# Optimization experiments

Measured on AMD Instinct MI355X. Metric: run time of the kernel, lower is better.

The kernel has to match this reference:

```python
import jax, jax.numpy as jnp
import numpy as np
import math

B, S, IN, D, H, L, DFF = 8, 512, 32, 512, 8, 6, 2048
DK = D // H
LN_EPS = 1e-5
KL_EPS = 1e-8


def _pos_encoding(seq_len, d_model):
    pe = np.zeros((seq_len, d_model), dtype=np.float32)
    pos = np.arange(seq_len, dtype=np.float32)[:, None]
    div = np.exp(np.arange(0, d_model, 2, dtype=np.float32) * (-math.log(10000.0) / d_model))
    pe[:, 0::2] = np.sin(pos * div)
    pe[:, 1::2] = np.cos(pos * div)
    return jnp.asarray(pe)


def setup_inputs() -> dict:
    key = jax.random.key(0)
    ks = iter(jax.random.split(key, 32))
    g = lambda shape: jax.random.normal(next(ks), shape, dtype=jnp.float32) * 0.02
    return {
        'x': jax.random.normal(next(ks), (B, S, IN), dtype=jnp.float32),
        'W_in': g((IN, D)), 'b_in': jnp.zeros((D,), jnp.float32),
        'pe': _pos_encoding(S, D),
        'Wq': g((L, D, D)), 'Wk': g((L, D, D)), 'Wv': g((L, D, D)),
        'Wo': g((L, D, D)), 'bo': jnp.zeros((L, D), jnp.float32),
        'W1': g((L, D, DFF)), 'b1': jnp.zeros((L, DFF), jnp.float32),
        'W2': g((L, DFF, D)), 'b2': jnp.zeros((L, D), jnp.float32),
        'ln1_g': jnp.ones((L, D), jnp.float32), 'ln1_b': jnp.zeros((L, D), jnp.float32),
        'ln2_g': jnp.ones((L, D), jnp.float32), 'ln2_b': jnp.zeros((L, D), jnp.float32),
        'W_out': g((D, IN)), 'b_out': jnp.zeros((IN,), jnp.float32),
        'Ws1': g((D, D // 2)), 'bs1': jnp.zeros((D // 2,), jnp.float32),
        'Ws2': g((D // 2, 1)), 'bs2': jnp.zeros((1,), jnp.float32),
    }


def _layernorm(v, gamma, beta):
    mu = v.mean(-1, keepdims=True)
    var = ((v - mu) ** 2).mean(-1, keepdims=True)
    return (v - mu) * jax.lax.rsqrt(var + LN_EPS) * gamma + beta


def reference(x, W_in, b_in, pe, Wq, Wk, Wv, Wo, bo, W1, b1, W2, b2,
              ln1_g, ln1_b, ln2_g, ln2_b, W_out, b_out, Ws1, bs1, Ws2, bs2):
    b, s, _ = x.shape
    h = x @ W_in + b_in + pe[None, :s, :]
    total_assoc = jnp.zeros((b, s), x.dtype)
    scale = 1.0 / math.sqrt(DK)
    prior = 1.0 / s + KL_EPS
    for l in range(L):
        # QKV: [b, h, s, dk]
        Q = (h @ Wq[l]).reshape(b, s, H, DK).transpose(0, 2, 1, 3)
        K = (h @ Wk[l]).reshape(b, s, H, DK).transpose(0, 2, 1, 3)
        V = (h @ Wv[l]).reshape(b, s, H, DK).transpose(0, 2, 1, 3)
        scores = jnp.einsum('bhsk,bhtk->bhst', Q, K) * scale
        attn = jax.nn.softmax(scores, axis=-1)  # [b,h,s,s]
        ctx = jnp.einsum('bhst,bhtk->bhsk', attn, V)
        ctx = ctx.transpose(0, 2, 1, 3).reshape(b, s, D)
        attn_out = ctx @ Wo[l] + bo[l]
        # association discrepancy: KL(avg_attn || uniform prior) per query
        avg_attn = attn.mean(axis=1) + KL_EPS  # [b,s,s]
        total_assoc = total_assoc + (avg_attn * jnp.log(avg_attn / prior)).sum(-1)
        h = _layernorm(h + attn_out, ln1_g[l], ln1_b[l])
        ff = jax.nn.relu(h @ W1[l] + b1[l]) @ W2[l] + b2[l]
        h = _layernorm(h + ff, ln2_g[l], ln2_b[l])
    reconstruction = h @ W_out + b_out
    anomaly_scores = jax.nn.sigmoid(jax.nn.relu(h @ Ws1 + bs1) @ Ws2 + bs2)[..., 0]
    avg_association = total_assoc / L
    return reconstruction, anomaly_scores, avg_association
```

## Files before the change

kernel.cpp:

```cpp
#include <hip/hip_runtime.h>
#include <math.h>

typedef __attribute__((ext_vector_type(8))) short bf16x8;
typedef __attribute__((ext_vector_type(4))) float f32x4;
typedef __attribute__((ext_vector_type(4))) float float4v;

__device__ __forceinline__ short f2bf(float v) {
  union { float f; unsigned u; } x; x.f = v;
  unsigned r = x.u + 0x7fffu + ((x.u >> 16) & 1u);
  return (short)(r >> 16);
}

__device__ __forceinline__ float bf2f(unsigned short u) {
  union { unsigned u; float f; } x; x.u = ((unsigned)u) << 16;
  return x.f;
}

__device__ __forceinline__ void gld_lds16(const void* g, void* l) {
  __builtin_amdgcn_global_load_lds((const __attribute__((address_space(1))) void*)g,
                                   (__attribute__((address_space(3))) void*)l, 16, 0, 0);
}

__global__ __launch_bounds__(256) void transpose_bf(const float* __restrict__ src,
                                                    short* __restrict__ dst,
                                                    int R, int C, size_t sStride, size_t dStride) {
  __shared__ float t[32][33];
  src += blockIdx.z * sStride;
  dst += blockIdx.z * dStride;
  int tx = threadIdx.x & 31, ty = threadIdx.x >> 5;
  int c0 = blockIdx.x * 32, r0 = blockIdx.y * 32;
#pragma unroll
  for (int i = 0; i < 4; i++)
    t[ty + i * 8][tx] = src[(size_t)(r0 + ty + i * 8) * C + c0 + tx];
  __syncthreads();
#pragma unroll
  for (int i = 0; i < 4; i++)
    dst[(size_t)(c0 + ty + i * 8) * R + r0 + tx] = f2bf(t[tx][ty + i * 8]);
}

__global__ __launch_bounds__(256) void transpose_qkv(const float* __restrict__ Wq,
                                                     const float* __restrict__ Wk,
                                                     const float* __restrict__ Wv,
                                                     short* __restrict__ qkvt) {
  __shared__ float t[32][33];
  const int z = blockIdx.z;
  const int which = z / 6, l = z % 6;
  const float* src = (which == 0 ? Wq : which == 1 ? Wk : Wv) + (size_t)l * 262144;
  short* dst = qkvt + (size_t)l * 786432 + (size_t)which * 262144;
  int tx = threadIdx.x & 31, ty = threadIdx.x >> 5;
  int c0 = blockIdx.x * 32, r0 = blockIdx.y * 32;
#pragma unroll
  for (int i = 0; i < 4; i++)
    t[ty + i * 8][tx] = src[(size_t)(r0 + ty + i * 8) * 512 + c0 + tx];
  __syncthreads();
#pragma unroll
  for (int i = 0; i < 4; i++)
    dst[(size_t)(c0 + ty + i * 8) * 512 + r0 + tx] = f2bf(t[tx][ty + i * 8]);
}

__global__ void embed_kernel(const float* __restrict__ x, const float* __restrict__ W_in,
                             const float* __restrict__ b_in, const float* __restrict__ pe,
                             float* __restrict__ h, short* __restrict__ hbf) {
  int col = (blockIdx.x & 1) * 256 + threadIdx.x;
  int row = blockIdx.x >> 1;
  int s = row & 511;
  float a = b_in[col] + pe[s * 512 + col];
  const float* xr = x + (size_t)row * 32;
#pragma unroll
  for (int k = 0; k < 32; k++) a += xr[k] * W_in[k * 512 + col];
  h[(size_t)row * 512 + col] = a;
  hbf[(size_t)row * 512 + col] = f2bf(a);
}

template <int EPI, int BM, int BN, int BK>
__global__ __launch_bounds__(256) void gemm_bt(const short* __restrict__ A,
                                               const short* __restrict__ Bt,
                                               float* __restrict__ Cf, short* __restrict__ Cb,
                                               const float* __restrict__ bias,
                                               int M, int N, int K) {
  __shared__ short As[BM * BK];
  __shared__ short Bs[BN * BK];
  const int tid = threadIdx.x;
  const int wid = tid >> 6;
  const int lane = tid & 63;
  const int m0 = blockIdx.y * BM;
  const int n0 = blockIdx.x * BN;
  constexpr int WR = BM / 2, WC = BN / 2, FI = WR / 16, FJ = WC / 16, KK = BK / 32;
  const int wr = (wid >> 1) * WR;
  const int wc = (wid & 1) * WC;

  f32x4 acc[FI][FJ];
#pragma unroll
  for (int i = 0; i < FI; i++)
#pragma unroll
    for (int j = 0; j < FJ; j++)
#pragma unroll
      for (int q = 0; q < 4; q++) acc[i][j][q] = 0.0f;

  const short* aBase = A + (size_t)m0 * K;
  const short* bBase = Bt + (size_t)n0 * K;
  constexpr int RPC = 512 / BK;
  constexpr int CA = BM / RPC;
  constexpr int CT = (BM + BN) / RPC;
  const int rowL = lane / (64 / RPC);
  const int colE = (lane % (64 / RPC)) * 8;
  const int kg = (lane >> 4) * 8;
  const int r16 = lane & 15;

  for (int kt = 0; kt < K; kt += BK) {
    __syncthreads();
#pragma unroll
    for (int c = 0; c < CT / 4; ++c) {
      int s = c * 4 + wid;
      if (s < CA)
        gld_lds16(aBase + (size_t)(s * RPC + rowL) * K + kt + colE, As + s * 512);
      else
        gld_lds16(bBase + (size_t)((s - CA) * RPC + rowL) * K + kt + colE, Bs + (s - CA) * 512);
    }
    __syncthreads();
    bf16x8 af[FI][KK], bfr[FJ][KK];
#pragma unroll
    for (int i = 0; i < FI; i++)
#pragma unroll
      for (int kk = 0; kk < KK; kk++)
        af[i][kk] = *(const bf16x8*)&As[(wr + i * 16 + r16) * BK + kk * 32 + kg];
#pragma unroll
    for (int j = 0; j < FJ; j++)
#pragma unroll
      for (int kk = 0; kk < KK; kk++)
        bfr[j][kk] = *(const bf16x8*)&Bs[(wc + j * 16 + r16) * BK + kk * 32 + kg];
#pragma unroll
    for (int kk = 0; kk < KK; kk++)
#pragma unroll
      for (int i = 0; i < FI; i++)
#pragma unroll
        for (int j = 0; j < FJ; j++)
          acc[i][j] = __builtin_amdgcn_mfma_f32_16x16x32_bf16(af[i][kk], bfr[j][kk], acc[i][j], 0, 0, 0);
  }

  const int col16 = lane & 15;
  const int rowg = (lane >> 4) * 4;
#pragma unroll
  for (int i = 0; i < FI; i++) {
    int row = m0 + wr + i * 16 + rowg;
#pragma unroll
    for (int j = 0; j < FJ; j++) {
      int col = n0 + wc + j * 16 + col16;
      float bv = (EPI == 1 || EPI == 2 || EPI == 4) ? bias[col] : 0.0f;
#pragma unroll
      for (int q = 0; q < 4; q++) {
        float v = acc[i][j][q] + bv;
        if (EPI == 2) {
          v = fmaxf(v, 0.0f);
          Cb[(size_t)(row + q) * N + col] = f2bf(v);
        } else if (EPI == 5) {
          int rr = row + q;
          int sect = col >> 9, hh = (col >> 6) & 7, dk = col & 63;
          int bq = rr >> 9, tt = rr & 511;
          Cb[(((size_t)(sect * 64 + bq * 8 + hh)) * 512 + tt) * 64 + dk] = f2bf(v);
        } else if (EPI == 3 || EPI == 4) {
          Cb[(size_t)(row + q) * N + col] = f2bf(v);
        } else {
          Cf[(size_t)(row + q) * N + col] = v;
        }
      }
    }
  }
}

__global__ __launch_bounds__(256) void vt_kernel(const short* __restrict__ qh,
                                                 short* __restrict__ Vt) {
  __shared__ short t[32][34];
  const int bh = blockIdx.z;
  const int t0 = blockIdx.x * 32, d0 = blockIdx.y * 32;
  const int tx = threadIdx.x & 31, ty = threadIdx.x >> 5;
  const short* Vh = qh + (size_t)(128 + bh) * 512 * 64;
#pragma unroll
  for (int i = 0; i < 4; i++)
    t[ty + i * 8][tx] = Vh[(size_t)(t0 + ty + i * 8) * 64 + d0 + tx];
  __syncthreads();
#pragma unroll
  for (int i = 0; i < 4; i++)
    Vt[((size_t)bh * 64 + d0 + ty + i * 8) * 512 + t0 + tx] = t[tx][ty + i * 8];
}

__global__ __launch_bounds__(256) void smpv_kernel(const short* __restrict__ qh,
                                                   const short* __restrict__ Vt,
                                                   short* __restrict__ P,
                                                   short* __restrict__ ctxb) {
  __shared__ short Pl[32 * 512];
  __shared__ float red0[2][2][16];
  __shared__ float red1[2][2][16];
  const int bh = blockIdx.y, b = bh >> 3, h = bh & 7;
  const int q0 = blockIdx.x * 32;
  const int tid = threadIdx.x;
  const int wid = tid >> 6, lane = tid & 63;
  const int r16 = lane & 15, g = lane >> 4;
  const int qh_ = wid & 1, th_ = wid >> 1;

  const short* Qh = qh + ((size_t)bh * 512) * 64;
  const short* Kh = qh + ((size_t)(64 + bh) * 512) * 64;

  const short* qp = Qh + (size_t)(q0 + qh_ * 16 + r16) * 64 + g * 8;
  const bf16x8 qa0 = *(const bf16x8*)qp;
  const bf16x8 qa1 = *(const bf16x8*)(qp + 32);

  f32x4 acc[16];
#pragma unroll
  for (int tt = 0; tt < 16; ++tt) {
    const short* kp = Kh + (size_t)(th_ * 256 + tt * 16 + r16) * 64 + g * 8;
    bf16x8 kb0 = *(const bf16x8*)kp;
    bf16x8 kb1 = *(const bf16x8*)(kp + 32);
    f32x4 c = {0.f, 0.f, 0.f, 0.f};
    c = __builtin_amdgcn_mfma_f32_16x16x32_bf16(qa0, kb0, c, 0, 0, 0);
    c = __builtin_amdgcn_mfma_f32_16x16x32_bf16(qa1, kb1, c, 0, 0, 0);
    acc[tt] = c;
  }

  float mx[4] = {-1e30f, -1e30f, -1e30f, -1e30f};
#pragma unroll
  for (int tt = 0; tt < 16; ++tt)
#pragma unroll
    for (int r = 0; r < 4; ++r) mx[r] = fmaxf(mx[r], acc[tt][r]);
#pragma unroll
  for (int r = 0; r < 4; ++r)
#pragma unroll
    for (int m = 8; m; m >>= 1) mx[r] = fmaxf(mx[r], __shfl_xor(mx[r], m, 16));
  if (r16 == 0) {
#pragma unroll
    for (int r = 0; r < 4; ++r) red0[th_][qh_][g * 4 + r] = mx[r];
  }
  __syncthreads();
#pragma unroll
  for (int r = 0; r < 4; ++r) {
    int q = g * 4 + r;
    mx[r] = fmaxf(red0[0][qh_][q], red0[1][qh_][q]);
  }
  float sum[4] = {0.f, 0.f, 0.f, 0.f};
#pragma unroll
  for (int tt = 0; tt < 16; ++tt)
#pragma unroll
    for (int r = 0; r < 4; ++r) {
      float e = __expf((acc[tt][r] - mx[r]) * 0.125f);
      acc[tt][r] = e;
      sum[r] += e;
    }
#pragma unroll
  for (int r = 0; r < 4; ++r)
#pragma unroll
    for (int m = 8; m; m >>= 1) sum[r] += __shfl_xor(sum[r], m, 16);
  if (r16 == 0) {
#pragma unroll
    for (int r = 0; r < 4; ++r) red1[th_][qh_][g * 4 + r] = sum[r];
  }
  __syncthreads();

  char* plc = (char*)Pl;
#pragma unroll
  for (int r = 0; r < 4; ++r) {
    int q = qh_ * 16 + g * 4 + r;
    float inv = 1.0f / (red1[0][qh_][g * 4 + r] + red1[1][qh_][g * 4 + r]);
    int swz = (q & 7) << 4;
#pragma unroll
    for (int tt = 0; tt < 16; ++tt)
      *(short*)(plc + q * 1024 + (((th_ * 256 + tt * 16 + r16) * 2) ^ swz)) =
          f2bf(acc[tt][r] * inv);
  }
  __syncthreads();

  short* pg = P + ((size_t)bh * 512 + q0) * 512;
#pragma unroll
  for (int rr = 0; rr < 8; ++rr) {
    int q = wid * 8 + rr;
    bf16x8 v = *(const bf16x8*)(plc + q * 1024 + ((lane * 16) ^ ((q & 7) << 4)));
    *(bf16x8*)&pg[(size_t)q * 512 + lane * 8] = v;
  }

  f32x4 pacc[2];
#pragma unroll
  for (int j = 0; j < 2; ++j)
#pragma unroll
    for (int q = 0; q < 4; ++q) pacc[j][q] = 0.f;
  const short* vb = Vt + (size_t)bh * 64 * 512 + (size_t)(th_ * 32) * 512;
  const int qr = qh_ * 16 + r16;
  const int rswz = (qr & 7) << 4;
  for (int kt = 0; kt < 512; kt += 32) {
    bf16x8 af = *(const bf16x8*)(plc + qr * 1024 + (((kt + g * 8) * 2) ^ rswz));
#pragma unroll
    for (int j = 0; j < 2; ++j) {
      bf16x8 bfr = *(const bf16x8*)&vb[(size_t)(j * 16 + r16) * 512 + kt + g * 8];
      pacc[j] = __builtin_amdgcn_mfma_f32_16x16x32_bf16(af, bfr, pacc[j], 0, 0, 0);
    }
  }
#pragma unroll
  for (int j = 0; j < 2; ++j) {
    int col = h * 64 + th_ * 32 + j * 16 + r16;
#pragma unroll
    for (int q = 0; q < 4; ++q)
      ctxb[(size_t)(b * 512 + q0 + qh_ * 16 + g * 4 + q) * 512 + col] = f2bf(pacc[j][q]);
  }
}

template <int FIRST>
__global__ __launch_bounds__(256) void kl_kernel(const short* __restrict__ P,
                                                 float* __restrict__ assoc) {
  const int wid = threadIdx.x >> 6, lane = threadIdx.x & 63;
  const int row = blockIdx.x * 4 + wid;
  const int b = row >> 9, q = row & 511;
  const float prior = 1.0f / 512.0f + 1e-8f;
  float hs[8] = {0.f, 0.f, 0.f, 0.f, 0.f, 0.f, 0.f, 0.f};
#pragma unroll
  for (int h = 0; h < 8; ++h) {
    bf16x8 v = *(const bf16x8*)&P[(((size_t)(b * 8 + h)) * 512 + q) * 512 + lane * 8];
#pragma unroll
    for (int k = 0; k < 8; ++k) hs[k] += bf2f((unsigned short)v[k]);
  }
  float s = 0.f;
#pragma unroll
  for (int k = 0; k < 8; ++k) {
    float a = hs[k] * 0.125f + 1e-8f;
    s += a * __logf(a / prior);
  }
#pragma unroll
  for (int m = 32; m; m >>= 1) s += __shfl_xor(s, m, 64);
  if (lane == 0) assoc[row] = FIRST ? s : (assoc[row] + s);
}

__global__ __launch_bounds__(256) void ln_kernel(const float* __restrict__ hin,
                                                 const short* __restrict__ res,
                                                 const float* __restrict__ g,
                                                 const float* __restrict__ bta,
                                                 float* __restrict__ hout, short* __restrict__ hbf) {
  const int wid = threadIdx.x >> 6, lane = threadIdx.x & 63;
  const size_t row = (size_t)blockIdx.x * 4 + wid;
  const float* hp = hin + row * 512 + lane * 8;
  float4v a0 = *(const float4v*)hp;
  float4v a1 = *(const float4v*)(hp + 4);
  bf16x8 rv = *(const bf16x8*)(res + row * 512 + lane * 8);
  float v[8], s = 0.f, s2 = 0.f;
#pragma unroll
  for (int i = 0; i < 8; i++) {
    float base = (i < 4) ? a0[i] : a1[i - 4];
    v[i] = base + bf2f((unsigned short)rv[i]);
    s += v[i];
    s2 += v[i] * v[i];
  }
#pragma unroll
  for (int m = 32; m; m >>= 1) {
    s += __shfl_xor(s, m, 64);
    s2 += __shfl_xor(s2, m, 64);
  }
  float mu = s * (1.0f / 512.0f);
  float var = s2 * (1.0f / 512.0f) - mu * mu;
  float rs = rsqrtf(var + 1e-5f);
  const float* gp = g + lane * 8;
  const float* bp = bta + lane * 8;
  float4v o0, o1;
  bf16x8 ob;
#pragma unroll
  for (int i = 0; i < 8; i++) {
    float y = (v[i] - mu) * rs * gp[i] + bp[i];
    if (i < 4) o0[i] = y; else o1[i - 4] = y;
    ob[i] = f2bf(y);
  }
  float* op = hout + row * 512 + lane * 8;
  *(float4v*)op = o0;
  *(float4v*)(op + 4) = o1;
  *(bf16x8*)(hbf + row * 512 + lane * 8) = ob;
}

__global__ __launch_bounds__(256) void recon_mfma(const short* __restrict__ hbf,
                                                  const short* __restrict__ WoutT,
                                                  const float* __restrict__ bout,
                                                  float* __restrict__ out) {
  const int wid = threadIdx.x >> 6, lane = threadIdx.x & 63;
  const int r16 = lane & 15, kg = (lane >> 4) * 8;
  const int wbase = blockIdx.x * 128 + wid * 32;

  f32x4 acc[2][2];
#pragma unroll
  for (int i = 0; i < 2; i++)
#pragma unroll
    for (int j = 0; j < 2; j++)
#pragma unroll
      for (int q = 0; q < 4; q++) acc[i][j][q] = 0.0f;

  for (int kt = 0; kt < 512; kt += 32) {
    bf16x8 af[2], bfr[2];
#pragma unroll
    for (int i = 0; i < 2; i++)
      af[i] = *(const bf16x8*)&hbf[(size_t)(wbase + i * 16 + r16) * 512 + kt + kg];
#pragma unroll
    for (int j = 0; j < 2; j++)
      bfr[j] = *(const bf16x8*)&WoutT[(size_t)(j * 16 + r16) * 512 + kt + kg];
#pragma unroll
    for (int i = 0; i < 2; i++)
#pragma unroll
      for (int j = 0; j < 2; j++)
        acc[i][j] = __builtin_amdgcn_mfma_f32_16x16x32_bf16(af[i], bfr[j], acc[i][j], 0, 0, 0);
  }

  const int rowg = (lane >> 4) * 4;
#pragma unroll
  for (int i = 0; i < 2; i++)
#pragma unroll
    for (int j = 0; j < 2; j++) {
      int col = j * 16 + r16;
#pragma unroll
      for (int q = 0; q < 4; q++)
        out[(size_t)(wbase + i * 16 + rowg + q) * 32 + col] = acc[i][j][q] + bout[col];
    }
}

__global__ __launch_bounds__(256) void score2_kernel(const short* __restrict__ s1,
                                                     const float* __restrict__ Ws2,
                                                     const float* __restrict__ bs2,
                                                     const float* __restrict__ assoc,
                                                     float* __restrict__ outScore,
                                                     float* __restrict__ outAssoc) {
  const int wid = threadIdx.x >> 6, lane = threadIdx.x & 63;
  const int row = blockIdx.x * 4 + wid;
  const short* rp = &s1[(size_t)row * 256 + lane * 4];
  float d = 0.f;
#pragma unroll
  for (int e = 0; e < 4; e++) d += bf2f((unsigned short)rp[e]) * Ws2[lane * 4 + e];
#pragma unroll
  for (int m = 32; m; m >>= 1) d += __shfl_xor(d, m, 64);
  if (lane == 0) {
    outScore[row] = 1.f / (1.f + __expf(-(d + bs2[0])));
    outAssoc[row] = assoc[row] * (1.0f / 6.0f);
  }
}

extern "C" void kernel_launch(void* const* d_in, const int* in_sizes, int n_in,
                              void* d_out, int out_size, void* d_ws, size_t ws_size,
                              hipStream_t stream) {
  const float* x    = (const float*)d_in[0];
  const float* W_in = (const float*)d_in[1];
  const float* b_in = (const float*)d_in[2];
  const float* pe   = (const float*)d_in[3];
  const float* Wq   = (const float*)d_in[4];
  const float* Wk   = (const float*)d_in[5];
  const float* Wv   = (const float*)d_in[6];
  const float* Wo   = (const float*)d_in[7];
  const float* bo   = (const float*)d_in[8];
  const float* W1   = (const float*)d_in[9];
  const float* b1   = (const float*)d_in[10];
  const float* W2   = (const float*)d_in[11];
  const float* b2   = (const float*)d_in[12];
  const float* ln1g = (const float*)d_in[13];
  const float* ln1b = (const float*)d_in[14];
  const float* ln2g = (const float*)d_in[15];
  const float* ln2b = (const float*)d_in[16];
  const float* Wout = (const float*)d_in[17];
  const float* bout = (const float*)d_in[18];
  const float* Ws1  = (const float*)d_in[19];
  const float* bs1  = (const float*)d_in[20];
  const float* Ws2  = (const float*)d_in[21];
  const float* bs2  = (const float*)d_in[22];

  char* p = (char*)d_ws;
  auto alloc = [&](size_t bytes) {
    void* r = (void*)p;
    p += (bytes + 255) & ~(size_t)255;
    return r;
  };
  float* h     = (float*)alloc((size_t)4096 * 512 * 4);
  short* h_bf  = (short*)alloc((size_t)4096 * 512 * 2);
  short* qh    = (short*)alloc((size_t)4096 * 1536 * 2);
  short* aout  = (short*)alloc((size_t)4096 * 512 * 2);
  short* ctxb  = (short*)alloc((size_t)4096 * 512 * 2);
  short* ff1b  = (short*)alloc((size_t)4096 * 2048 * 2);
  short* ff2   = (short*)alloc((size_t)4096 * 512 * 2);
  float* assoc = (float*)alloc((size_t)4096 * 4);
  short* Pbuf  = (short*)alloc((size_t)64 * 512 * 512 * 2);
  short* Vt    = (short*)alloc((size_t)64 * 64 * 512 * 2);
  short* sc1   = (short*)alloc((size_t)4096 * 256 * 2);
  short* qkvt  = (short*)alloc((size_t)6 * 1536 * 512 * 2);
  short* wot   = (short*)alloc((size_t)6 * 512 * 512 * 2);
  short* w1t   = (short*)alloc((size_t)6 * 2048 * 512 * 2);
  short* w2t   = (short*)alloc((size_t)6 * 512 * 2048 * 2);
  short* ws1t  = (short*)alloc((size_t)256 * 512 * 2);
  short* woutT = (short*)alloc((size_t)32 * 512 * 2);

  transpose_qkv<<<dim3(16, 16, 18), 256, 0, stream>>>(Wq, Wk, Wv, qkvt);
  transpose_bf<<<dim3(16, 16, 6), 256, 0, stream>>>(Wo, wot, 512, 512, 262144, 262144);
  transpose_bf<<<dim3(64, 16, 6), 256, 0, stream>>>(W1, w1t, 512, 2048, 1048576, 1048576);
  transpose_bf<<<dim3(16, 64, 6), 256, 0, stream>>>(W2, w2t, 2048, 512, 1048576, 1048576);
  transpose_bf<<<dim3(8, 16, 1), 256, 0, stream>>>(Ws1, ws1t, 512, 256, 0, 0);
  transpose_bf<<<dim3(1, 16, 1), 256, 0, stream>>>(Wout, woutT, 512, 32, 0, 0);

  embed_kernel<<<8192, 256, 0, stream>>>(x, W_in, b_in, pe, h, h_bf);

  for (int l = 0; l < 6; ++l) {
    gemm_bt<5, 128, 128, 32><<<dim3(12, 32), 256, 0, stream>>>(
        h_bf, qkvt + (size_t)l * 786432, nullptr, qh, nullptr, 4096, 1536, 512);
    vt_kernel<<<dim3(16, 2, 64), 256, 0, stream>>>(qh, Vt);
    smpv_kernel<<<dim3(16, 64), 256, 0, stream>>>(qh, Vt, Pbuf, ctxb);
    if (l == 0)
      kl_kernel<1><<<1024, 256, 0, stream>>>(Pbuf, assoc);
    else
      kl_kernel<0><<<1024, 256, 0, stream>>>(Pbuf, assoc);
    gemm_bt<4, 64, 64, 32><<<dim3(8, 64), 256, 0, stream>>>(
        ctxb, wot + (size_t)l * 262144, nullptr, aout, bo + l * 512, 4096, 512, 512);
    ln_kernel<<<1024, 256, 0, stream>>>(h, aout, ln1g + l * 512, ln1b + l * 512, h, h_bf);
    gemm_bt<2, 128, 128, 32><<<dim3(16, 32), 256, 0, stream>>>(
        h_bf, w1t + (size_t)l * 1048576, nullptr, ff1b, b1 + l * 2048, 4096, 2048, 512);
    gemm_bt<4, 64, 64, 32><<<dim3(8, 64), 256, 0, stream>>>(
        ff1b, w2t + (size_t)l * 1048576, nullptr, ff2, b2 + l * 512, 4096, 512, 2048);
    ln_kernel<<<1024, 256, 0, stream>>>(h, ff2, ln2g + l * 512, ln2b + l * 512, h, h_bf);
  }

  float* out = (float*)d_out;
  recon_mfma<<<32, 256, 0, stream>>>(h_bf, woutT, bout, out);
  gemm_bt<2, 128, 128, 32><<<dim3(2, 32), 256, 0, stream>>>(h_bf, ws1t, nullptr, sc1, bs1,
                                                            4096, 256, 512);
  score2_kernel<<<1024, 256, 0, stream>>>(sc1, Ws2, bs2, assoc, out + 131072,
                                          out + 131072 + 4096);
}
```

Baseline: 864.7 us.

## Fuse prologue kernels, merge Wo GEMM with KL, drop fp32 residual stream

Merges all weight transposes and the embedding into one prologue launch, and runs the Wo projection GEMM and the KL association reduction as two block ranges of a single launch. The fp32 hidden-state copy is removed, so the residual and LayerNorm now read and write only the bf16 hidden buffer. The goal is fewer launches and less memory traffic. In exchange, residual accumulation happens in bf16 across six layers, which may reduce accuracy.

```diff
diff --git a/kernel.cpp b/kernel.cpp
--- a/kernel.cpp
+++ b/kernel.cpp
@@ -3,7 +3,6 @@
 
 typedef __attribute__((ext_vector_type(8))) short bf16x8;
 typedef __attribute__((ext_vector_type(4))) float f32x4;
-typedef __attribute__((ext_vector_type(4))) float float4v;
 
 __device__ __forceinline__ short f2bf(float v) {
   union { float f; unsigned u; } x; x.f = v;
@@ -21,14 +20,68 @@
                                    (__attribute__((address_space(3))) void*)l, 16, 0, 0);
 }
 
-__global__ __launch_bounds__(256) void transpose_bf(const float* __restrict__ src,
-                                                    short* __restrict__ dst,
-                                                    int R, int C, size_t sStride, size_t dStride) {
+__global__ __launch_bounds__(256) void prologue_kernel(
+    const float* __restrict__ x, const float* __restrict__ W_in, const float* __restrict__ b_in,
+    const float* __restrict__ pe, short* __restrict__ hbf,
+    const float* __restrict__ Wq, const float* __restrict__ Wk, const float* __restrict__ Wv,
+    const float* __restrict__ Wo, const float* __restrict__ W1, const float* __restrict__ W2,
+    const float* __restrict__ Ws1, const float* __restrict__ Wout,
+    short* __restrict__ qkvt, short* __restrict__ wot, short* __restrict__ w1t,
+    short* __restrict__ w2t, short* __restrict__ ws1t, short* __restrict__ woutT) {
   __shared__ float t[32][33];
-  src += blockIdx.z * sStride;
-  dst += blockIdx.z * dStride;
-  int tx = threadIdx.x & 31, ty = threadIdx.x >> 5;
-  int c0 = blockIdx.x * 32, r0 = blockIdx.y * 32;
+  const int tid = threadIdx.x;
+  int idx = blockIdx.x;
+  if (idx < 8192) {
+    int col = (idx & 1) * 256 + tid;
+    int row = idx >> 1;
+    int s = row & 511;
+    float a = b_in[col] + pe[s * 512 + col];
+    const float* xr = x + (size_t)row * 32;
+#pragma unroll
+    for (int k = 0; k < 32; k++) a += xr[k] * W_in[k * 512 + col];
+    hbf[(size_t)row * 512 + col] = f2bf(a);
+    return;
+  }
+  idx -= 8192;
+  const float* src;
+  short* dst;
+  int R, C, cx, cy;
+  if (idx < 4608) {
+    int z = idx >> 8, rem = idx & 255;
+    cx = rem & 15; cy = rem >> 4;
+    int which = z / 6, l = z % 6;
+    src = (which == 0 ? Wq : which == 1 ? Wk : Wv) + (size_t)l * 262144;
+    dst = qkvt + (size_t)l * 786432 + (size_t)which * 262144;
+    R = 512; C = 512;
+  } else if (idx < 6144) {
+    int j = idx - 4608;
+    int l = j >> 8, rem = j & 255;
+    cx = rem & 15; cy = rem >> 4;
+    src = Wo + (size_t)l * 262144; dst = wot + (size_t)l * 262144;
+    R = 512; C = 512;
+  } else if (idx < 12288) {
+    int j = idx - 6144;
+    int l = j >> 10, rem = j & 1023;
+    cx = rem & 63; cy = rem >> 6;
+    src = W1 + (size_t)l * 1048576; dst = w1t + (size_t)l * 1048576;
+    R = 512; C = 2048;
+  } else if (idx < 18432) {
+    int j = idx - 12288;
+    int l = j >> 10, rem = j & 1023;
+    cx = rem & 15; cy = rem >> 4;
+    src = W2 + (size_t)l * 1048576; dst = w2t + (size_t)l * 1048576;
+    R = 2048; C = 512;
+  } else if (idx < 18560) {
+    int j = idx - 18432;
+    cx = j & 7; cy = j >> 3;
+    src = Ws1; dst = ws1t; R = 512; C = 256;
+  } else {
+    int j = idx - 18560;
+    cx = 0; cy = j;
+    src = Wout; dst = woutT; R = 512; C = 32;
+  }
+  const int tx = tid & 31, ty = tid >> 5;
+  const int c0 = cx * 32, r0 = cy * 32;
 #pragma unroll
   for (int i = 0; i < 4; i++)
     t[ty + i * 8][tx] = src[(size_t)(r0 + ty + i * 8) * C + c0 + tx];
@@ -38,44 +91,10 @@
     dst[(size_t)(c0 + ty + i * 8) * R + r0 + tx] = f2bf(t[tx][ty + i * 8]);
 }
 
-__global__ __launch_bounds__(256) void transpose_qkv(const float* __restrict__ Wq,
-                                                     const float* __restrict__ Wk,
-                                                     const float* __restrict__ Wv,
-                                                     short* __restrict__ qkvt) {
-  __shared__ float t[32][33];
-  const int z = blockIdx.z;
-  const int which = z / 6, l = z % 6;
-  const float* src = (which == 0 ? Wq : which == 1 ? Wk : Wv) + (size_t)l * 262144;
-  short* dst = qkvt + (size_t)l * 786432 + (size_t)which * 262144;
-  int tx = threadIdx.x & 31, ty = threadIdx.x >> 5;
-  int c0 = blockIdx.x * 32, r0 = blockIdx.y * 32;
-#pragma unroll
-  for (int i = 0; i < 4; i++)
-    t[ty + i * 8][tx] = src[(size_t)(r0 + ty + i * 8) * 512 + c0 + tx];
-  __syncthreads();
-#pragma unroll
-  for (int i = 0; i < 4; i++)
-    dst[(size_t)(c0 + ty + i * 8) * 512 + r0 + tx] = f2bf(t[tx][ty + i * 8]);
-}
-
-__global__ void embed_kernel(const float* __restrict__ x, const float* __restrict__ W_in,
-                             const float* __restrict__ b_in, const float* __restrict__ pe,
-                             float* __restrict__ h, short* __restrict__ hbf) {
-  int col = (blockIdx.x & 1) * 256 + threadIdx.x;
-  int row = blockIdx.x >> 1;
-  int s = row & 511;
-  float a = b_in[col] + pe[s * 512 + col];
-  const float* xr = x + (size_t)row * 32;
-#pragma unroll
-  for (int k = 0; k < 32; k++) a += xr[k] * W_in[k * 512 + col];
-  h[(size_t)row * 512 + col] = a;
-  hbf[(size_t)row * 512 + col] = f2bf(a);
-}
-
 template <int EPI, int BM, int BN, int BK>
 __global__ __launch_bounds__(256) void gemm_bt(const short* __restrict__ A,
                                                const short* __restrict__ Bt,
-                                               float* __restrict__ Cf, short* __restrict__ Cb,
+                                               short* __restrict__ Cb,
                                                const float* __restrict__ bias,
                                                int M, int N, int K) {
   __shared__ short As[BM * BK];
@@ -146,7 +165,7 @@
 #pragma unroll
     for (int j = 0; j < FJ; j++) {
       int col = n0 + wc + j * 16 + col16;
-      float bv = (EPI == 1 || EPI == 2 || EPI == 4) ? bias[col] : 0.0f;
+      float bv = (EPI == 2 || EPI == 4) ? bias[col] : 0.0f;
 #pragma unroll
       for (int q = 0; q < 4; q++) {
         float v = acc[i][j][q] + bv;
@@ -158,10 +177,8 @@
           int sect = col >> 9, hh = (col >> 6) & 7, dk = col & 63;
           int bq = rr >> 9, tt = rr & 511;
           Cb[(((size_t)(sect * 64 + bq * 8 + hh)) * 512 + tt) * 64 + dk] = f2bf(v);
-        } else if (EPI == 3 || EPI == 4) {
+        } else {
           Cb[(size_t)(row + q) * N + col] = f2bf(v);
-        } else {
-          Cf[(size_t)(row + q) * N + col] = v;
         }
       }
     }
@@ -302,46 +319,108 @@
 }
 
 template <int FIRST>
-__global__ __launch_bounds__(256) void kl_kernel(const short* __restrict__ P,
-                                                 float* __restrict__ assoc) {
-  const int wid = threadIdx.x >> 6, lane = threadIdx.x & 63;
-  const int row = blockIdx.x * 4 + wid;
-  const int b = row >> 9, q = row & 511;
-  const float prior = 1.0f / 512.0f + 1e-8f;
-  float hs[8] = {0.f, 0.f, 0.f, 0.f, 0.f, 0.f, 0.f, 0.f};
-#pragma unroll
-  for (int h = 0; h < 8; ++h) {
-    bf16x8 v = *(const bf16x8*)&P[(((size_t)(b * 8 + h)) * 512 + q) * 512 + lane * 8];
-#pragma unroll
-    for (int k = 0; k < 8; ++k) hs[k] += bf2f((unsigned short)v[k]);
-  }
-  float s = 0.f;
-#pragma unroll
-  for (int k = 0; k < 8; ++k) {
-    float a = hs[k] * 0.125f + 1e-8f;
-    s += a * __logf(a / prior);
-  }
-#pragma unroll
-  for (int m = 32; m; m >>= 1) s += __shfl_xor(s, m, 64);
-  if (lane == 0) assoc[row] = FIRST ? s : (assoc[row] + s);
-}
-
-__global__ __launch_bounds__(256) void ln_kernel(const float* __restrict__ hin,
-                                                 const short* __restrict__ res,
+__global__ __launch_bounds__(256) void wo_kl_kernel(const short* __restrict__ A,
+                                                    const short* __restrict__ Bt,
+                                                    const float* __restrict__ bias,
+                                                    short* __restrict__ aout,
+                                                    const short* __restrict__ P,
+                                                    float* __restrict__ assoc) {
+  __shared__ short As[64 * 32];
+  __shared__ short Bs[64 * 32];
+  const int tid = threadIdx.x;
+  const int wid = tid >> 6, lane = tid & 63;
+  if (blockIdx.x < 8) {
+    const int m0 = blockIdx.y * 64;
+    const int n0 = blockIdx.x * 64;
+    const int wr = (wid >> 1) * 32;
+    const int wc = (wid & 1) * 32;
+    f32x4 acc[2][2];
+#pragma unroll
+    for (int i = 0; i < 2; i++)
+#pragma unroll
+      for (int j = 0; j < 2; j++)
+#pragma unroll
+        for (int q = 0; q < 4; q++) acc[i][j][q] = 0.0f;
+    const short* aBase = A + (size_t)m0 * 512;
+    const short* bBase = Bt + (size_t)n0 * 512;
+    const int rowL = lane >> 2;
+    const int colE = (lane & 3) * 8;
+    const int kg = (lane >> 4) * 8;
+    const int r16 = lane & 15;
+    for (int kt = 0; kt < 512; kt += 32) {
+      __syncthreads();
+#pragma unroll
+      for (int c = 0; c < 2; ++c) {
+        int s = c * 4 + wid;
+        if (s < 4)
+          gld_lds16(aBase + (size_t)(s * 16 + rowL) * 512 + kt + colE, As + s * 512);
+        else
+          gld_lds16(bBase + (size_t)((s - 4) * 16 + rowL) * 512 + kt + colE, Bs + (s - 4) * 512);
+      }
+      __syncthreads();
+      bf16x8 af[2], bfr[2];
+#pragma unroll
+      for (int i = 0; i < 2; i++)
+        af[i] = *(const bf16x8*)&As[(wr + i * 16 + r16) * 32 + kg];
+#pragma unroll
+      for (int j = 0; j < 2; j++)
+        bfr[j] = *(const bf16x8*)&Bs[(wc + j * 16 + r16) * 32 + kg];
+#pragma unroll
+      for (int i = 0; i < 2; i++)
+#pragma unroll
+        for (int j = 0; j < 2; j++)
+          acc[i][j] = __builtin_amdgcn_mfma_f32_16x16x32_bf16(af[i], bfr[j], acc[i][j], 0, 0, 0);
+    }
+    const int col16 = lane & 15;
+    const int rowg = (lane >> 4) * 4;
+#pragma unroll
+    for (int i = 0; i < 2; i++) {
+      int row = m0 + wr + i * 16 + rowg;
+#pragma unroll
+      for (int j = 0; j < 2; j++) {
+        int col = n0 + wc + j * 16 + col16;
+        float bv = bias[col];
+#pragma unroll
+        for (int q = 0; q < 4; q++)
+          aout[(size_t)(row + q) * 512 + col] = f2bf(acc[i][j][q] + bv);
+      }
+    }
+  } else {
+    const int kb = (blockIdx.x - 8) * 64 + blockIdx.y;
+    const int row = kb * 4 + wid;
+    const int b = row >> 9, q = row & 511;
+    const float prior = 1.0f / 512.0f + 1e-8f;
+    float hs[8] = {0.f, 0.f, 0.f, 0.f, 0.f, 0.f, 0.f, 0.f};
+#pragma unroll
+    for (int h = 0; h < 8; ++h) {
+      bf16x8 v = *(const bf16x8*)&P[(((size_t)(b * 8 + h)) * 512 + q) * 512 + lane * 8];
+#pragma unroll
+      for (int k = 0; k < 8; ++k) hs[k] += bf2f((unsigned short)v[k]);
+    }
+    float s = 0.f;
+#pragma unroll
+    for (int k = 0; k < 8; ++k) {
+      float a = hs[k] * 0.125f + 1e-8f;
+      s += a * __logf(a / prior);
+    }
+#pragma unroll
+    for (int m = 32; m; m >>= 1) s += __shfl_xor(s, m, 64);
+    if (lane == 0) assoc[row] = FIRST ? s : (assoc[row] + s);
+  }
+}
+
+__global__ __launch_bounds__(256) void ln_kernel(const short* __restrict__ res,
                                                  const float* __restrict__ g,
                                                  const float* __restrict__ bta,
-                                                 float* __restrict__ hout, short* __restrict__ hbf) {
+                                                 short* __restrict__ hbf) {
   const int wid = threadIdx.x >> 6, lane = threadIdx.x & 63;
   const size_t row = (size_t)blockIdx.x * 4 + wid;
-  const float* hp = hin + row * 512 + lane * 8;
-  float4v a0 = *(const float4v*)hp;
-  float4v a1 = *(const float4v*)(hp + 4);
-  bf16x8 rv = *(const bf16x8*)(res + row * 512 + lane * 8);
+  bf16x8 hv = *(const bf16x8*)&hbf[row * 512 + lane * 8];
+  bf16x8 rv = *(const bf16x8*)&res[row * 512 + lane * 8];
   float v[8], s = 0.f, s2 = 0.f;
 #pragma unroll
   for (int i = 0; i < 8; i++) {
-    float base = (i < 4) ? a0[i] : a1[i - 4];
-    v[i] = base + bf2f((unsigned short)rv[i]);
+    v[i] = bf2f((unsigned short)hv[i]) + bf2f((unsigned short)rv[i]);
     s += v[i];
     s2 += v[i] * v[i];
   }
@@ -355,18 +434,10 @@
   float rs = rsqrtf(var + 1e-5f);
   const float* gp = g + lane * 8;
   const float* bp = bta + lane * 8;
-  float4v o0, o1;
   bf16x8 ob;
 #pragma unroll
-  for (int i = 0; i < 8; i++) {
-    float y = (v[i] - mu) * rs * gp[i] + bp[i];
-    if (i < 4) o0[i] = y; else o1[i - 4] = y;
-    ob[i] = f2bf(y);
-  }
-  float* op = hout + row * 512 + lane * 8;
-  *(float4v*)op = o0;
-  *(float4v*)(op + 4) = o1;
-  *(bf16x8*)(hbf + row * 512 + lane * 8) = ob;
+  for (int i = 0; i < 8; i++) ob[i] = f2bf((v[i] - mu) * rs * gp[i] + bp[i]);
+  *(bf16x8*)&hbf[row * 512 + lane * 8] = ob;
 }
 
 __global__ __launch_bounds__(256) void recon_mfma(const short* __restrict__ hbf,
@@ -465,7 +536,6 @@
     p += (bytes + 255) & ~(size_t)255;
     return r;
   };
-  float* h     = (float*)alloc((size_t)4096 * 512 * 4);
   short* h_bf  = (short*)alloc((size_t)4096 * 512 * 2);
   short* qh    = (short*)alloc((size_t)4096 * 1536 * 2);
   short* aout  = (short*)alloc((size_t)4096 * 512 * 2);
@@ -483,37 +553,31 @@
   short* ws1t  = (short*)alloc((size_t)256 * 512 * 2);
   short* woutT = (short*)alloc((size_t)32 * 512 * 2);
 
-  transpose_qkv<<<dim3(16, 16, 18), 256, 0, stream>>>(Wq, Wk, Wv, qkvt);
-  transpose_bf<<<dim3(16, 16, 6), 256, 0, stream>>>(Wo, wot, 512, 512, 262144, 262144);
-  transpose_bf<<<dim3(64, 16, 6), 256, 0, stream>>>(W1, w1t, 512, 2048, 1048576, 1048576);
-  transpose_bf<<<dim3(16, 64, 6), 256, 0, stream>>>(W2, w2t, 2048, 512, 1048576, 1048576);
-  transpose_bf<<<dim3(8, 16, 1), 256, 0, stream>>>(Ws1, ws1t, 512, 256, 0, 0);
-  transpose_bf<<<dim3(1, 16, 1), 256, 0, stream>>>(Wout, woutT, 512, 32, 0, 0);
-
-  embed_kernel<<<8192, 256, 0, stream>>>(x, W_in, b_in, pe, h, h_bf);
+  prologue_kernel<<<26768, 256, 0, stream>>>(x, W_in, b_in, pe, h_bf, Wq, Wk, Wv, Wo, W1, W2,
+                                             Ws1, Wout, qkvt, wot, w1t, w2t, ws1t, woutT);
 
   for (int l = 0; l < 6; ++l) {
     gemm_bt<5, 128, 128, 32><<<dim3(12, 32), 256, 0, stream>>>(
-        h_bf, qkvt + (size_t)l * 786432, nullptr, qh, nullptr, 4096, 1536, 512);
+        h_bf, qkvt + (size_t)l * 786432, qh, nullptr, 4096, 1536, 512);
     vt_kernel<<<dim3(16, 2, 64), 256, 0, stream>>>(qh, Vt);
     smpv_kernel<<<dim3(16, 64), 256, 0, stream>>>(qh, Vt, Pbuf, ctxb);
     if (l == 0)
-      kl_kernel<1><<<1024, 256, 0, stream>>>(Pbuf, assoc);
+      wo_kl_kernel<1><<<dim3(24, 64), 256, 0, stream>>>(ctxb, wot + (size_t)l * 262144,
+                                                        bo + l * 512, aout, Pbuf, assoc);
     else
-      kl_kernel<0><<<1024, 256, 0, stream>>>(Pbuf, assoc);
+      wo_kl_kernel<0><<<dim3(24, 64), 256, 0, stream>>>(ctxb, wot + (size_t)l * 262144,
+                                                        bo + l * 512, aout, Pbuf, assoc);
+    ln_kernel<<<1024, 256, 0, stream>>>(aout, ln1g + l * 512, ln1b + l * 512, h_bf);
+    gemm_bt<2, 128, 128, 32><<<dim3(16, 32), 256, 0, stream>>>(
+        h_bf, w1t + (size_t)l * 1048576, ff1b, b1 + l * 2048, 4096, 2048, 512);
     gemm_bt<4, 64, 64, 32><<<dim3(8, 64), 256, 0, stream>>>(
-        ctxb, wot + (size_t)l * 262144, nullptr, aout, bo + l * 512, 4096, 512, 512);
-    ln_kernel<<<1024, 256, 0, stream>>>(h, aout, ln1g + l * 512, ln1b + l * 512, h, h_bf);
-    gemm_bt<2, 128, 128, 32><<<dim3(16, 32), 256, 0, stream>>>(
-        h_bf, w1t + (size_t)l * 1048576, nullptr, ff1b, b1 + l * 2048, 4096, 2048, 512);
-    gemm_bt<4, 64, 64, 32><<<dim3(8, 64), 256, 0, stream>>>(
-        ff1b, w2t + (size_t)l * 1048576, nullptr, ff2, b2 + l * 512, 4096, 512, 2048);
-    ln_kernel<<<1024, 256, 0, stream>>>(h, ff2, ln2g + l * 512, ln2b + l * 512, h, h_bf);
+        ff1b, w2t + (size_t)l * 1048576, ff2, b2 + l * 512, 4096, 512, 2048);
+    ln_kernel<<<1024, 256, 0, stream>>>(ff2, ln2g + l * 512, ln2b + l * 512, h_bf);
   }
 
   float* out = (float*)d_out;
   recon_mfma<<<32, 256, 0, stream>>>(h_bf, woutT, bout, out);
-  gemm_bt<2, 128, 128, 32><<<dim3(2, 32), 256, 0, stream>>>(h_bf, ws1t, nullptr, sc1, bs1,
+  gemm_bt<2, 128, 128, 32><<<dim3(2, 32), 256, 0, stream>>>(h_bf, ws1t, sc1, bs1,
                                                             4096, 256, 512);
   score2_kernel<<<1024, 256, 0, stream>>>(sc1, Ws2, bs2, assoc, out + 131072,
                                           out + 131072 + 4096);
```

Result: faster. 801.3 us (-7.3%).
